# Kernel tuning notes

Measured on AMD Instinct MI355X. Metric: run time of the kernel, lower is better.

## Reference

```python
import jax, jax.numpy as jnp
import numpy as np

N_NODES = 65536
N_EDGES = 524288
IN_CH = 128
FHC = 256      # first_hc = max(hidden, in)
HID = 256
NCLS = 3
NODES_PER_GRAPH = 32


def setup_inputs() -> dict:
    key = jax.random.key(0)
    ks = jax.random.split(key, 16)
    s = 1.0 / np.sqrt(FHC)
    inp = {
        "x": jax.random.normal(ks[0], (N_NODES, IN_CH), dtype=jnp.float32),
        "edge_index": jax.random.randint(ks[1], (2, N_EDGES), 0, N_NODES, dtype=jnp.int64),
        "edge_attr": jax.random.uniform(ks[2], (N_EDGES,), dtype=jnp.float32),
        # GatedGraphConv params: per-layer matmul weight + GRUCell
        "gg_w": jax.random.uniform(ks[3], (2, FHC, FHC), minval=-s, maxval=s, dtype=jnp.float32),
        "w_ih": jax.random.uniform(ks[4], (3 * FHC, FHC), minval=-s, maxval=s, dtype=jnp.float32),
        "w_hh": jax.random.uniform(ks[5], (3 * FHC, FHC), minval=-s, maxval=s, dtype=jnp.float32),
        "b_ih": jax.random.uniform(ks[6], (3 * FHC,), minval=-s, maxval=s, dtype=jnp.float32),
        "b_hh": jax.random.uniform(ks[7], (3 * FHC,), minval=-s, maxval=s, dtype=jnp.float32),
        # Conv1d(FHC, 1, kernel_size=1)
        "cnn_w": jax.random.uniform(ks[8], (1, FHC, 1), minval=-s, maxval=s, dtype=jnp.float32),
        "cnn_b": jax.random.uniform(ks[9], (1,), minval=-s, maxval=s, dtype=jnp.float32),
        # Linear(32, HID), Linear(HID, NCLS)
        "lin1_w": jax.random.uniform(ks[10], (HID, NODES_PER_GRAPH), minval=-0.17, maxval=0.17, dtype=jnp.float32),
        "lin1_b": jax.random.uniform(ks[11], (HID,), minval=-0.17, maxval=0.17, dtype=jnp.float32),
        "lin2_w": jax.random.uniform(ks[12], (NCLS, HID), minval=-s, maxval=s, dtype=jnp.float32),
        "lin2_b": jax.random.uniform(ks[13], (NCLS,), minval=-s, maxval=s, dtype=jnp.float32),
    }
    return inp


def _gated_graph_conv(x, src, dst, edge_w, gg_w, w_ih, w_hh, b_ih, b_hh):
    # PyG GatedGraphConv: pad input to out_channels, then num_layers iterations.
    n = x.shape[0]
    h = jnp.pad(x, ((0, 0), (0, FHC - x.shape[1])))  # [N, FHC]
    for i in range(2):
        m = h @ gg_w[i]                                   # [N, FHC]
        msgs = m[src] * edge_w[:, None]                   # gather per edge [E, FHC]
        agg = jax.ops.segment_sum(msgs, dst, num_segments=n)  # scatter-add [N, FHC]
        # GRUCell(input=agg, hidden=h), torch gate order: r, z, n
        gi = agg @ w_ih.T + b_ih
        gh = h @ w_hh.T + b_hh
        ir, iz, ig = jnp.split(gi, 3, axis=1)
        hr, hz, hg = jnp.split(gh, 3, axis=1)
        r = jax.nn.sigmoid(ir + hr)
        z = jax.nn.sigmoid(iz + hz)
        g = jnp.tanh(ig + r * hg)
        h = (1.0 - z) * g + z * h
    return h


def reference(x, edge_index, edge_attr, gg_w, w_ih, w_hh, b_ih, b_hh,
              cnn_w, cnn_b, lin1_w, lin1_b, lin2_w, lin2_b):
    src, dst = edge_index[0], edge_index[1]
    h = _gated_graph_conv(x, src, dst, edge_attr, gg_w, w_ih, w_hh, b_ih, b_hh)
    h = jax.nn.relu(h)  # dropout is identity in eval mode
    bs = h.shape[0] // NODES_PER_GRAPH
    h = h.reshape(bs, NODES_PER_GRAPH, FHC)          # (bs e) f -> bs e f
    # Conv1d(FHC,1,k=1) over layout (bs, f, e): y[b,e] = sum_f w[0,f,0]*h[b,e,f] + b
    y = jnp.einsum('bef,f->be', h, cnn_w[:, :, 0].reshape(FHC)) + cnn_b[0]
    y = jax.nn.relu(y)                               # [bs, 32]
    y = y @ lin1_w.T + lin1_b
    y = jax.nn.relu(y)
    y = y @ lin2_w.T + lin2_b
    return jax.nn.softmax(y, axis=-1)
```

## Files before the change

kernel.cpp:

```cpp
#include <hip/hip_runtime.h>
#include <math.h>

#define N_NODES 65536
#define N_EDGES 524288
#define IN_CH 128
#define FHC 256
#define NCLS 3
#define NPG 32
#define NGRAPH (N_NODES / NPG)

typedef __attribute__((ext_vector_type(8))) short bfrag;
typedef __attribute__((ext_vector_type(4))) float facc;

__device__ inline float sigmoidf_(float x) { return 1.0f / (1.0f + expf(-x)); }

__device__ __forceinline__ float fast_sigmoid(float x) {
    return __builtin_amdgcn_rcpf(1.0f + __expf(-x));
}
__device__ __forceinline__ float fast_tanh(float x) {
    return 1.0f - 2.0f * __builtin_amdgcn_rcpf(__expf(2.0f * x) + 1.0f);
}

__device__ inline short f2bf(float f) {
    union { float f; unsigned u; } v; v.f = f;
    unsigned r = v.u + 0x7fffu + ((v.u >> 16) & 1u);
    return (short)(r >> 16);
}
__device__ inline float bf2f(short s) {
    union { unsigned u; float f; } v; v.u = ((unsigned)(unsigned short)s) << 16;
    return v.f;
}

__device__ __forceinline__ void gld16(const short* g, short* l) {
    __builtin_amdgcn_global_load_lds(
        (const __attribute__((address_space(1))) void*)g,
        (__attribute__((address_space(3))) void*)l, 16, 0, 0);
}

__global__ void convert_kernel(const float* __restrict__ gg_w, const float* __restrict__ wih,
                               const float* __restrict__ whh, short* __restrict__ ggT,
                               short* __restrict__ wih16, short* __restrict__ whh16) {
    int t = blockIdx.x * 256 + threadIdx.x;
    if (t < 2 * FHC * FHC) {
        int i = t >> 16, r = t & 65535, n = r >> 8, k = r & 255;
        ggT[t] = f2bf(gg_w[i * FHC * FHC + k * FHC + n]);
    } else if (t < 2 * FHC * FHC + 3 * FHC * FHC) {
        int u = t - 2 * FHC * FHC;
        wih16[u] = f2bf(wih[u]);
    } else {
        int u = t - 5 * FHC * FHC;
        whh16[u] = f2bf(whh[u]);
    }
}

__global__ void pad16_kernel(const float* __restrict__ x, short* __restrict__ h) {
    int idx = blockIdx.x * 256 + threadIdx.x;
    int c4 = idx & 63, n = idx >> 6;
    short4 v = {0, 0, 0, 0};
    if (c4 < 32) {
        float4 xv = reinterpret_cast<const float4*>(x)[n * 32 + c4];
        v.x = f2bf(xv.x); v.y = f2bf(xv.y); v.z = f2bf(xv.z); v.w = f2bf(xv.w);
    }
    reinterpret_cast<short4*>(h)[idx] = v;
}

__global__ void hist_kernel(const int* __restrict__ ei, int* __restrict__ deg) {
    int e = blockIdx.x * 256 + threadIdx.x;
    atomicAdd(&deg[ei[N_EDGES + e]], 1);
}

__global__ void scan_reduce_kernel(const int* __restrict__ deg, int* __restrict__ bsum) {
    __shared__ int s[256];
    int t = threadIdx.x;
    s[t] = deg[blockIdx.x * 256 + t];
    __syncthreads();
    for (int off = 128; off > 0; off >>= 1) {
        if (t < off) s[t] += s[t + off];
        __syncthreads();
    }
    if (t == 0) bsum[blockIdx.x] = s[0];
}

__global__ void scan_bsum_kernel(const int* __restrict__ bsum, int* __restrict__ boff) {
    __shared__ int s[256];
    int t = threadIdx.x;
    int v = bsum[t];
    s[t] = v;
    __syncthreads();
    for (int off = 1; off < 256; off <<= 1) {
        int u = (t >= off) ? s[t - off] : 0;
        __syncthreads();
        s[t] += u;
        __syncthreads();
    }
    boff[t] = s[t] - v;
}

__global__ void scan_write_kernel(const int* __restrict__ deg, const int* __restrict__ boff,
                                  int* __restrict__ rowptr, int* __restrict__ cur) {
    __shared__ int s[256];
    int t = threadIdx.x, gid = blockIdx.x * 256 + t;
    int v = deg[gid];
    s[t] = v;
    __syncthreads();
    for (int off = 1; off < 256; off <<= 1) {
        int u = (t >= off) ? s[t - off] : 0;
        __syncthreads();
        s[t] += u;
        __syncthreads();
    }
    int excl = boff[blockIdx.x] + s[t] - v;
    rowptr[gid] = excl;
    cur[gid] = excl;
    if (gid == N_NODES - 1) rowptr[N_NODES] = excl + v;
}

__global__ void fill_kernel(const int* __restrict__ ei, const float* __restrict__ ea,
                            int* __restrict__ cur, int2* __restrict__ csr) {
    int e = blockIdx.x * 256 + threadIdx.x;
    int dst = ei[N_EDGES + e];
    int pos = atomicAdd(&cur[dst], 1);
    csr[pos] = make_int2(ei[e], __float_as_int(ea[e]));
}

__global__ __launch_bounds__(256) void gather_kernel(const short* __restrict__ m,
                                                     const int* __restrict__ rowptr,
                                                     const int2* __restrict__ csr,
                                                     short* __restrict__ agg16) {
    int node = blockIdx.x * 4 + (threadIdx.x >> 6);
    int lane = threadIdx.x & 63;
    int beg = rowptr[node], end = rowptr[node + 1];
    const short4* m4 = reinterpret_cast<const short4*>(m);
    float a0 = 0.f, a1 = 0.f, a2 = 0.f, a3 = 0.f;
#define GSTEP(E)                                            \
    {                                                       \
        float w = __int_as_float((E).y);                    \
        short4 v = m4[(size_t)(E).x * 64 + lane];           \
        a0 += bf2f(v.x) * w;                                \
        a1 += bf2f(v.y) * w;                                \
        a2 += bf2f(v.z) * w;                                \
        a3 += bf2f(v.w) * w;                                \
    }
    int j = beg;
    for (; j + 8 <= end; j += 8) {
        int2 e0 = csr[j + 0], e1 = csr[j + 1], e2 = csr[j + 2], e3 = csr[j + 3];
        int2 e4 = csr[j + 4], e5 = csr[j + 5], e6 = csr[j + 6], e7 = csr[j + 7];
        GSTEP(e0) GSTEP(e1) GSTEP(e2) GSTEP(e3)
        GSTEP(e4) GSTEP(e5) GSTEP(e6) GSTEP(e7)
    }
    for (; j + 2 <= end; j += 2) {
        int2 e0 = csr[j + 0], e1 = csr[j + 1];
        GSTEP(e0) GSTEP(e1)
    }
    if (j < end) {
        int2 e0 = csr[j];
        GSTEP(e0)
    }
#undef GSTEP
    short4 o;
    o.x = f2bf(a0); o.y = f2bf(a1); o.z = f2bf(a2); o.w = f2bf(a3);
    reinterpret_cast<short4*>(agg16)[(size_t)node * 64 + lane] = o;
}

__global__ __launch_bounds__(256, 2) void mgemm_kernel(const short* __restrict__ A,
                                                       const short* __restrict__ W,
                                                       short* __restrict__ C) {
    __shared__ __align__(16) short lds[3 * 16 * 512];
    int tid = threadIdx.x;
    int lane = tid & 63, wv = tid >> 6, fr = lane & 15, fc = lane >> 4;
    int m0 = blockIdx.x * 128, n0 = blockIdx.y * 128;
    int srow = lane >> 2;
    int scol = (lane & 3) ^ ((lane >> 3) & 3);
    const short* gsrc[4];
    int ldsoff[4];
#pragma unroll
    for (int i = 0; i < 4; ++i) {
        int ch = wv * 4 + i;
        if (ch < 8) {
            ldsoff[i] = ch * 512;
            gsrc[i] = A + (size_t)(m0 + ch * 16 + srow) * FHC + scol * 8;
        } else {
            ldsoff[i] = 4096 + (ch - 8) * 512;
            gsrc[i] = W + (size_t)(n0 + (ch - 8) * 16 + srow) * FHC + scol * 8;
        }
    }
    int fcs = fc ^ ((fr >> 1) & 3);

    auto STAGE = [&](int ks, int bufsel) {
        short* dst = &lds[bufsel * 8192];
#pragma unroll
        for (int i = 0; i < 4; ++i) gld16(gsrc[i] + ks * 32, dst + ldsoff[i]);
    };

    facc acc[2][8] = {};
    STAGE(0, 0);
    STAGE(1, 1);
    for (int ks = 0; ks < 8; ++ks) {
        if (ks < 7) { asm volatile("s_waitcnt vmcnt(4)" ::: "memory"); }
        else        { asm volatile("s_waitcnt vmcnt(0)" ::: "memory"); }
        __builtin_amdgcn_sched_barrier(0);
        __builtin_amdgcn_s_barrier();
        __builtin_amdgcn_sched_barrier(0);
        if (ks + 2 < 8) STAGE(ks + 2, (ks + 2) % 3);
        __builtin_amdgcn_sched_barrier(0);
        const short* B = &lds[(ks % 3) * 8192];
        int ar = (wv * 32 + fr) * 32 + fcs * 8;
        bfrag a0 = *reinterpret_cast<const bfrag*>(B + ar);
        bfrag a1 = *reinterpret_cast<const bfrag*>(B + ar + 16 * 32);
        __builtin_amdgcn_s_setprio(1);
#pragma unroll
        for (int cf = 0; cf < 8; ++cf) {
            bfrag b = *reinterpret_cast<const bfrag*>(B + 4096 + (cf * 16 + fr) * 32 + fcs * 8);
            acc[0][cf] = __builtin_amdgcn_mfma_f32_16x16x32_bf16(a0, b, acc[0][cf], 0, 0, 0);
            acc[1][cf] = __builtin_amdgcn_mfma_f32_16x16x32_bf16(a1, b, acc[1][cf], 0, 0, 0);
        }
        __builtin_amdgcn_s_setprio(0);
    }
#pragma unroll
    for (int s = 0; s < 2; ++s)
#pragma unroll
        for (int cf = 0; cf < 8; ++cf)
#pragma unroll
            for (int r = 0; r < 4; ++r) {
                int node = m0 + wv * 32 + s * 16 + fc * 4 + r;
                int c = n0 + cf * 16 + fr;
                C[(size_t)node * FHC + c] = f2bf(acc[s][cf][r]);
            }
}

__global__ __launch_bounds__(256, 2) void gru_mfma_kernel(
    const short* __restrict__ agg16, const short* __restrict__ hin, short* __restrict__ hout,
    const short* __restrict__ wih16, const short* __restrict__ whh16,
    const float* __restrict__ bih, const float* __restrict__ bhh) {
    __shared__ __align__(16) short lds[3 * 16 * 512];
    int tid = threadIdx.x;
    int lane = tid & 63, wv = tid >> 6, fr = lane & 15, fc = lane >> 4;
    int c = blockIdx.y * 64 + wv * 16 + fr;

    bfrag wreg[6][8];
    {
        size_t roff = (size_t)c * FHC + fc * 8;
#pragma unroll
        for (int ks = 0; ks < 8; ++ks) {
            wreg[0][ks] = *reinterpret_cast<const bfrag*>(wih16 + roff + ks * 32);
            wreg[1][ks] = *reinterpret_cast<const bfrag*>(wih16 + (size_t)256 * FHC + roff + ks * 32);
            wreg[2][ks] = *reinterpret_cast<const bfrag*>(wih16 + (size_t)512 * FHC + roff + ks * 32);
            wreg[3][ks] = *reinterpret_cast<const bfrag*>(whh16 + roff + ks * 32);
            wreg[4][ks] = *reinterpret_cast<const bfrag*>(whh16 + (size_t)256 * FHC + roff + ks * 32);
            wreg[5][ks] = *reinterpret_cast<const bfrag*>(whh16 + (size_t)512 * FHC + roff + ks * 32);
        }
    }
    float br = bih[c] + bhh[c];
    float bz = bih[c + 256] + bhh[c + 256];
    float big = bih[c + 512], bhg = bhh[c + 512];

    int srow = lane >> 2;
    int scol = (lane & 3) ^ ((lane >> 3) & 3);
    const short* gb[4];
    int ldsoff[4];
#pragma unroll
    for (int i = 0; i < 4; ++i) {
        int ch = wv * 4 + i;
        int mat = ch >> 3, ks = ch & 7;
        const short* src = mat ? hin : agg16;
        gb[i] = src + (size_t)srow * FHC + ks * 32 + scol * 8;
        ldsoff[i] = ch * 512;
    }
    int fcs = fc ^ ((fr >> 1) & 3);
    int lo = (fr * 4 + fcs) * 8;
    const int NT = 32;
    int tile0 = blockIdx.x * NT;

    int hbase = (8 + (c >> 5)) * 512 + (c & 7);
    int hg = (c >> 3) & 3;

    auto STAGE = [&](int t, int bufsel) {
        size_t noff = (size_t)(tile0 + t) * 16 * FHC;
        short* dst = &lds[bufsel * 8192];
#pragma unroll
        for (int i = 0; i < 4; ++i) gld16(gb[i] + noff, dst + ldsoff[i]);
    };

    STAGE(0, 0);
    STAGE(1, 1);
    for (int t = 0; t < NT; ++t) {
        if (t == 0)                   { asm volatile("s_waitcnt vmcnt(4)" ::: "memory"); }
        else if (t == 1 || t == NT-1) { asm volatile("s_waitcnt vmcnt(8)" ::: "memory"); }
        else                          { asm volatile("s_waitcnt vmcnt(12)" ::: "memory"); }
        __builtin_amdgcn_sched_barrier(0);
        __builtin_amdgcn_s_barrier();
        __builtin_amdgcn_sched_barrier(0);
        if (t + 2 < NT) STAGE(t + 2, (t + 2) % 3);
        __builtin_amdgcn_sched_barrier(0);
        const short* B = &lds[(t % 3) * 8192];
        facc aR = {}, aZ = {}, aG = {}, aH = {};
        __builtin_amdgcn_s_setprio(1);
#pragma unroll
        for (int ks = 0; ks < 8; ++ks) {
            bfrag ag = *reinterpret_cast<const bfrag*>(B + ks * 512 + lo);
            bfrag hh = *reinterpret_cast<const bfrag*>(B + (8 + ks) * 512 + lo);
            aR = __builtin_amdgcn_mfma_f32_16x16x32_bf16(ag, wreg[0][ks], aR, 0, 0, 0);
            aR = __builtin_amdgcn_mfma_f32_16x16x32_bf16(hh, wreg[3][ks], aR, 0, 0, 0);
            aZ = __builtin_amdgcn_mfma_f32_16x16x32_bf16(ag, wreg[1][ks], aZ, 0, 0, 0);
            aZ = __builtin_amdgcn_mfma_f32_16x16x32_bf16(hh, wreg[4][ks], aZ, 0, 0, 0);
            aG = __builtin_amdgcn_mfma_f32_16x16x32_bf16(ag, wreg[2][ks], aG, 0, 0, 0);
            aH = __builtin_amdgcn_mfma_f32_16x16x32_bf16(hh, wreg[5][ks], aH, 0, 0, 0);
        }
        __builtin_amdgcn_s_setprio(0);
        int node0 = (tile0 + t) * 16;
#pragma unroll
        for (int r = 0; r < 4; ++r) {
            int row = fc * 4 + r;
            float hold = bf2f(B[hbase + (row * 4 + (hg ^ ((row >> 1) & 3))) * 8]);
            float rg = fast_sigmoid(aR[r] + br);
            float z = fast_sigmoid(aZ[r] + bz);
            float g = fast_tanh(aG[r] + big + rg * (aH[r] + bhg));
            hout[(size_t)(node0 + row) * FHC + c] = f2bf(g + z * (hold - g));
        }
    }
}

__global__ void cnn_kernel(const short* __restrict__ h, const float* __restrict__ w,
                           const float* __restrict__ b, float* __restrict__ y1) {
    int node = blockIdx.x * 4 + (threadIdx.x >> 6);
    int lane = threadIdx.x & 63;
    short4 hv = reinterpret_cast<const short4*>(h)[(size_t)node * 64 + lane];
    float4 wv = reinterpret_cast<const float4*>(w)[lane];
    float p = fmaxf(bf2f(hv.x), 0.f) * wv.x + fmaxf(bf2f(hv.y), 0.f) * wv.y +
              fmaxf(bf2f(hv.z), 0.f) * wv.z + fmaxf(bf2f(hv.w), 0.f) * wv.w;
#pragma unroll
    for (int off = 32; off > 0; off >>= 1) p += __shfl_down(p, off, 64);
    if (lane == 0) y1[node] = fmaxf(p + b[0], 0.f);
}

__global__ __launch_bounds__(256) void head_kernel(
    const float* __restrict__ y1, const float* __restrict__ l1w,
    const float* __restrict__ l1b, const float* __restrict__ l2w,
    const float* __restrict__ l2b, float* __restrict__ out) {
    __shared__ float ys[32];
    __shared__ float zs[256];
    __shared__ float os[3];
    int b = blockIdx.x, tid = threadIdx.x;
    if (tid < 32) ys[tid] = y1[b * 32 + tid];
    __syncthreads();
    float acc = l1b[tid];
#pragma unroll
    for (int k = 0; k < 32; ++k) acc += ys[k] * l1w[tid * 32 + k];
    zs[tid] = fmaxf(acc, 0.f);
    __syncthreads();
    int wave = tid >> 6, lane = tid & 63;
    if (wave < 3) {
        float p = 0.f;
#pragma unroll
        for (int j = 0; j < 4; ++j) p += zs[lane + j * 64] * l2w[wave * 256 + lane + j * 64];
#pragma unroll
        for (int off = 32; off > 0; off >>= 1) p += __shfl_down(p, off, 64);
        if (lane == 0) os[wave] = p + l2b[wave];
    }
    __syncthreads();
    if (tid == 0) {
        float mx = fmaxf(os[0], fmaxf(os[1], os[2]));
        float e0 = expf(os[0] - mx), e1 = expf(os[1] - mx), e2 = expf(os[2] - mx);
        float s = e0 + e1 + e2;
        out[b * 3 + 0] = e0 / s;
        out[b * 3 + 1] = e1 / s;
        out[b * 3 + 2] = e2 / s;
    }
}

extern "C" void kernel_launch(void* const* d_in, const int* in_sizes, int n_in,
                              void* d_out, int out_size, void* d_ws, size_t ws_size,
                              hipStream_t stream) {
    const float* x = (const float*)d_in[0];
    const int* ei = (const int*)d_in[1];
    const float* ea = (const float*)d_in[2];
    const float* gg_w = (const float*)d_in[3];
    const float* w_ih = (const float*)d_in[4];
    const float* w_hh = (const float*)d_in[5];
    const float* b_ih = (const float*)d_in[6];
    const float* b_hh = (const float*)d_in[7];
    const float* cnn_w = (const float*)d_in[8];
    const float* cnn_b = (const float*)d_in[9];
    const float* l1w = (const float*)d_in[10];
    const float* l1b = (const float*)d_in[11];
    const float* l2w = (const float*)d_in[12];
    const float* l2b = (const float*)d_in[13];
    float* out = (float*)d_out;

    const size_t nodeE = (size_t)N_NODES * FHC;
    char* p = (char*)d_ws;
    short* hA = (short*)p;      p += nodeE * 2;
    short* hB = (short*)p;      p += nodeE * 2;
    short* m16 = (short*)p;     p += nodeE * 2;
    short* agg16 = (short*)p;   p += nodeE * 2;
    short* ggT = (short*)p;     p += (size_t)2 * FHC * FHC * 2;
    short* wih16 = (short*)p;   p += (size_t)3 * FHC * FHC * 2;
    short* whh16 = (short*)p;   p += (size_t)3 * FHC * FHC * 2;
    float* y1 = (float*)p;      p += (size_t)N_NODES * 4;
    int* deg = (int*)p;         p += (size_t)N_NODES * 4;
    int* rowptr = (int*)p;      p += (size_t)(N_NODES + 4) * 4;
    int* cur = (int*)p;         p += (size_t)N_NODES * 4;
    int* bsum = (int*)p;        p += 256 * 4;
    int* boff = (int*)p;        p += 256 * 4;
    int2* csr = (int2*)p;       p += (size_t)N_EDGES * 8;

    dim3 grid_gemm(N_NODES / 128, FHC / 128);
    dim3 grid_gru(128, 4);

    convert_kernel<<<8 * FHC * FHC / 256, 256, 0, stream>>>(gg_w, w_ih, w_hh, ggT, wih16, whh16);
    pad16_kernel<<<N_NODES * 64 / 256, 256, 0, stream>>>(x, hA);

    hipMemsetAsync(deg, 0, (size_t)N_NODES * 4, stream);
    hist_kernel<<<N_EDGES / 256, 256, 0, stream>>>(ei, deg);
    scan_reduce_kernel<<<N_NODES / 256, 256, 0, stream>>>(deg, bsum);
    scan_bsum_kernel<<<1, 256, 0, stream>>>(bsum, boff);
    scan_write_kernel<<<N_NODES / 256, 256, 0, stream>>>(deg, boff, rowptr, cur);
    fill_kernel<<<N_EDGES / 256, 256, 0, stream>>>(ei, ea, cur, csr);

    mgemm_kernel<<<grid_gemm, 256, 0, stream>>>(hA, ggT, m16);
    gather_kernel<<<N_NODES / 4, 256, 0, stream>>>(m16, rowptr, csr, agg16);
    gru_mfma_kernel<<<grid_gru, 256, 0, stream>>>(agg16, hA, hB, wih16, whh16, b_ih, b_hh);

    mgemm_kernel<<<grid_gemm, 256, 0, stream>>>(hB, ggT + FHC * FHC, m16);
    gather_kernel<<<N_NODES / 4, 256, 0, stream>>>(m16, rowptr, csr, agg16);
    gru_mfma_kernel<<<grid_gru, 256, 0, stream>>>(agg16, hB, hA, wih16, whh16, b_ih, b_hh);

    cnn_kernel<<<N_NODES / 4, 256, 0, stream>>>(hA, cnn_w, cnn_b, y1);
    head_kernel<<<NGRAPH, 256, 0, stream>>>(y1, l1w, l1b, l2w, l2b, out);
}
```

Before: 319.7 us.

## Software-pipeline GRU epilogue with next tile's MFMA using ping-pong accumulators

The GRU tile loop is restructured so the gate nonlinearities and h stores for tile t-1 run after the MFMA chain for tile t, using two alternating accumulator sets. The aim is to hide transcendental math and global store latency behind matrix-core work. The old h values are read from LDS into registers during the current tile, so the buffer can be recycled. This costs extra VGPRs for the second accumulator set, retunes the vmcnt waits and drops the setprio hints.

```diff
diff --git a/kernel.cpp b/kernel.cpp
--- a/kernel.cpp
+++ b/kernel.cpp
@@ -281,41 +281,73 @@
         for (int i = 0; i < 4; ++i) gld16(gb[i] + noff, dst + ldsoff[i]);
     };
 
+    facc aR0 = {}, aZ0 = {}, aG0 = {}, aH0 = {};
+    facc aR1 = {}, aZ1 = {}, aG1 = {}, aH1 = {};
+    float hd0[4], hd1[4];
+    const facc FZ = {0.f, 0.f, 0.f, 0.f};
+
     STAGE(0, 0);
     STAGE(1, 1);
-    for (int t = 0; t < NT; ++t) {
-        if (t == 0)                   { asm volatile("s_waitcnt vmcnt(4)" ::: "memory"); }
-        else if (t == 1 || t == NT-1) { asm volatile("s_waitcnt vmcnt(8)" ::: "memory"); }
-        else                          { asm volatile("s_waitcnt vmcnt(12)" ::: "memory"); }
-        __builtin_amdgcn_sched_barrier(0);
-        __builtin_amdgcn_s_barrier();
-        __builtin_amdgcn_sched_barrier(0);
-        if (t + 2 < NT) STAGE(t + 2, (t + 2) % 3);
-        __builtin_amdgcn_sched_barrier(0);
-        const short* B = &lds[(t % 3) * 8192];
-        facc aR = {}, aZ = {}, aG = {}, aH = {};
-        __builtin_amdgcn_s_setprio(1);
-#pragma unroll
-        for (int ks = 0; ks < 8; ++ks) {
-            bfrag ag = *reinterpret_cast<const bfrag*>(B + ks * 512 + lo);
-            bfrag hh = *reinterpret_cast<const bfrag*>(B + (8 + ks) * 512 + lo);
-            aR = __builtin_amdgcn_mfma_f32_16x16x32_bf16(ag, wreg[0][ks], aR, 0, 0, 0);
-            aR = __builtin_amdgcn_mfma_f32_16x16x32_bf16(hh, wreg[3][ks], aR, 0, 0, 0);
-            aZ = __builtin_amdgcn_mfma_f32_16x16x32_bf16(ag, wreg[1][ks], aZ, 0, 0, 0);
-            aZ = __builtin_amdgcn_mfma_f32_16x16x32_bf16(hh, wreg[4][ks], aZ, 0, 0, 0);
-            aG = __builtin_amdgcn_mfma_f32_16x16x32_bf16(ag, wreg[2][ks], aG, 0, 0, 0);
-            aH = __builtin_amdgcn_mfma_f32_16x16x32_bf16(hh, wreg[5][ks], aH, 0, 0, 0);
-        }
-        __builtin_amdgcn_s_setprio(0);
-        int node0 = (tile0 + t) * 16;
+
+#define GRU_TILE(T, aRc, aZc, aGc, aHc, hdc, aRp, aZp, aGp, aHp, hdp, FIRST)                 \
+    do {                                                                                     \
+        int t_ = (T);                                                                        \
+        if (t_ <= 1)            { asm volatile("s_waitcnt vmcnt(4)" ::: "memory"); }         \
+        else if (t_ == 2)       { asm volatile("s_waitcnt vmcnt(8)" ::: "memory"); }         \
+        else if (t_ == NT - 1)  { asm volatile("s_waitcnt vmcnt(8)" ::: "memory"); }         \
+        else                    { asm volatile("s_waitcnt vmcnt(12)" ::: "memory"); }        \
+        __builtin_amdgcn_sched_barrier(0);                                                   \
+        __builtin_amdgcn_s_barrier();                                                        \
+        __builtin_amdgcn_sched_barrier(0);                                                   \
+        if (t_ + 2 < NT) STAGE(t_ + 2, (t_ + 2) % 3);                                        \
+        const short* B = &lds[(t_ % 3) * 8192];                                              \
+        aRc = FZ; aZc = FZ; aGc = FZ; aHc = FZ;                                              \
+        _Pragma("unroll")                                                                    \
+        for (int ks = 0; ks < 8; ++ks) {                                                     \
+            bfrag ag = *reinterpret_cast<const bfrag*>(B + ks * 512 + lo);                   \
+            bfrag hh = *reinterpret_cast<const bfrag*>(B + (8 + ks) * 512 + lo);             \
+            aRc = __builtin_amdgcn_mfma_f32_16x16x32_bf16(ag, wreg[0][ks], aRc, 0, 0, 0);    \
+            aRc = __builtin_amdgcn_mfma_f32_16x16x32_bf16(hh, wreg[3][ks], aRc, 0, 0, 0);    \
+            aZc = __builtin_amdgcn_mfma_f32_16x16x32_bf16(ag, wreg[1][ks], aZc, 0, 0, 0);    \
+            aZc = __builtin_amdgcn_mfma_f32_16x16x32_bf16(hh, wreg[4][ks], aZc, 0, 0, 0);    \
+            aGc = __builtin_amdgcn_mfma_f32_16x16x32_bf16(ag, wreg[2][ks], aGc, 0, 0, 0);    \
+            aHc = __builtin_amdgcn_mfma_f32_16x16x32_bf16(hh, wreg[5][ks], aHc, 0, 0, 0);    \
+        }                                                                                    \
+        _Pragma("unroll")                                                                    \
+        for (int r = 0; r < 4; ++r) {                                                        \
+            int row = fc * 4 + r;                                                            \
+            hdc[r] = bf2f(B[hbase + (row * 4 + (hg ^ ((row >> 1) & 3))) * 8]);               \
+        }                                                                                    \
+        if (!(FIRST)) {                                                                      \
+            int node0 = (tile0 + t_ - 1) * 16;                                               \
+            _Pragma("unroll")                                                                \
+            for (int r = 0; r < 4; ++r) {                                                    \
+                int row = fc * 4 + r;                                                        \
+                float rg = fast_sigmoid(aRp[r] + br);                                        \
+                float z = fast_sigmoid(aZp[r] + bz);                                         \
+                float g = fast_tanh(aGp[r] + big + rg * (aHp[r] + bhg));                     \
+                hout[(size_t)(node0 + row) * FHC + c] = f2bf(g + z * (hdp[r] - g));          \
+            }                                                                                \
+        }                                                                                    \
+        __builtin_amdgcn_sched_barrier(0);                                                   \
+    } while (0)
+
+    GRU_TILE(0, aR0, aZ0, aG0, aH0, hd0, aR1, aZ1, aG1, aH1, hd1, true);
+    GRU_TILE(1, aR1, aZ1, aG1, aH1, hd1, aR0, aZ0, aG0, aH0, hd0, false);
+    for (int tt = 2; tt < NT; tt += 2) {
+        GRU_TILE(tt, aR0, aZ0, aG0, aH0, hd0, aR1, aZ1, aG1, aH1, hd1, false);
+        GRU_TILE(tt + 1, aR1, aZ1, aG1, aH1, hd1, aR0, aZ0, aG0, aH0, hd0, false);
+    }
+#undef GRU_TILE
+    {
+        int node0 = (tile0 + NT - 1) * 16;
 #pragma unroll
         for (int r = 0; r < 4; ++r) {
             int row = fc * 4 + r;
-            float hold = bf2f(B[hbase + (row * 4 + (hg ^ ((row >> 1) & 3))) * 8]);
-            float rg = fast_sigmoid(aR[r] + br);
-            float z = fast_sigmoid(aZ[r] + bz);
-            float g = fast_tanh(aG[r] + big + rg * (aH[r] + bhg));
-            hout[(size_t)(node0 + row) * FHC + c] = f2bf(g + z * (hold - g));
+            float rg = fast_sigmoid(aR1[r] + br);
+            float z = fast_sigmoid(aZ1[r] + bz);
+            float g = fast_tanh(aG1[r] + big + rg * (aH1[r] + bhg));
+            hout[(size_t)(node0 + row) * FHC + c] = f2bf(g + z * (hd1[r] - g));
         }
     }
 }
```

Result: slower. 524.8 us (+64.1%).

## Fold message weight into GRU input weight and gather raw hidden states

Applied to the files above, without the earlier changes.

The code reassociates (A·(h·W))·W_ihᵀ as (A·h)·(W·W_ihᵀ). Two small weight products are precomputed once, so the per-node message GEMM and its intermediate buffer disappear from both layers. The gather now aggregates h directly, and the GRU kernel consumes the fused weight. The first layer runs a templated variant that only walks the 128 non-padded input channels, halving its K loop and staging. In exchange, the fused weight is rounded to bf16 once, so numerics differ slightly, and the code adds templated wait counts and special handling for the padded hidden columns.

```diff
diff --git a/kernel.cpp b/kernel.cpp
--- a/kernel.cpp
+++ b/kernel.cpp
@@ -12,8 +12,6 @@
 typedef __attribute__((ext_vector_type(8))) short bfrag;
 typedef __attribute__((ext_vector_type(4))) float facc;
 
-__device__ inline float sigmoidf_(float x) { return 1.0f / (1.0f + expf(-x)); }
-
 __device__ __forceinline__ float fast_sigmoid(float x) {
     return __builtin_amdgcn_rcpf(1.0f + __expf(-x));
 }
@@ -37,14 +35,23 @@
         (__attribute__((address_space(3))) void*)l, 16, 0, 0);
 }
 
+template <int N> __device__ __forceinline__ void vwait() {
+    if constexpr (N == 0)       asm volatile("s_waitcnt vmcnt(0)" ::: "memory");
+    else if constexpr (N == 2)  asm volatile("s_waitcnt vmcnt(2)" ::: "memory");
+    else if constexpr (N == 4)  asm volatile("s_waitcnt vmcnt(4)" ::: "memory");
+    else if constexpr (N == 6)  asm volatile("s_waitcnt vmcnt(6)" ::: "memory");
+    else if constexpr (N == 8)  asm volatile("s_waitcnt vmcnt(8)" ::: "memory");
+    else if constexpr (N == 10) asm volatile("s_waitcnt vmcnt(10)" ::: "memory");
+    else                        asm volatile("s_waitcnt vmcnt(12)" ::: "memory");
+}
+
 __global__ void convert_kernel(const float* __restrict__ gg_w, const float* __restrict__ wih,
-                               const float* __restrict__ whh, short* __restrict__ ggT,
+                               const float* __restrict__ whh, short* __restrict__ gg16,
                                short* __restrict__ wih16, short* __restrict__ whh16) {
     int t = blockIdx.x * 256 + threadIdx.x;
     if (t < 2 * FHC * FHC) {
-        int i = t >> 16, r = t & 65535, n = r >> 8, k = r & 255;
-        ggT[t] = f2bf(gg_w[i * FHC * FHC + k * FHC + n]);
-    } else if (t < 2 * FHC * FHC + 3 * FHC * FHC) {
+        gg16[t] = f2bf(gg_w[t]);
+    } else if (t < 5 * FHC * FHC) {
         int u = t - 2 * FHC * FHC;
         wih16[u] = f2bf(wih[u]);
     } else {
@@ -228,23 +235,27 @@
             }
 }
 
-__global__ __launch_bounds__(256, 2) void gru_mfma_kernel(
-    const short* __restrict__ agg16, const short* __restrict__ hin, short* __restrict__ hout,
-    const short* __restrict__ wih16, const short* __restrict__ whh16,
+template <int NKS>
+__global__ __launch_bounds__(256, 2) void gru_fused_kernel(
+    const short* __restrict__ hagg16, const short* __restrict__ hin, short* __restrict__ hout,
+    const short* __restrict__ wfT, const short* __restrict__ whh16,
     const float* __restrict__ bih, const float* __restrict__ bhh) {
-    __shared__ __align__(16) short lds[3 * 16 * 512];
+    constexpr int NCH = 2 * NKS;
+    constexpr int NL = NCH / 4;
+    constexpr int BUF = NCH * 512;
+    __shared__ __align__(16) short lds[3 * BUF];
     int tid = threadIdx.x;
     int lane = tid & 63, wv = tid >> 6, fr = lane & 15, fc = lane >> 4;
     int c = blockIdx.y * 64 + wv * 16 + fr;
 
-    bfrag wreg[6][8];
+    bfrag wreg[6][NKS];
     {
         size_t roff = (size_t)c * FHC + fc * 8;
 #pragma unroll
-        for (int ks = 0; ks < 8; ++ks) {
-            wreg[0][ks] = *reinterpret_cast<const bfrag*>(wih16 + roff + ks * 32);
-            wreg[1][ks] = *reinterpret_cast<const bfrag*>(wih16 + (size_t)256 * FHC + roff + ks * 32);
-            wreg[2][ks] = *reinterpret_cast<const bfrag*>(wih16 + (size_t)512 * FHC + roff + ks * 32);
+        for (int ks = 0; ks < NKS; ++ks) {
+            wreg[0][ks] = *reinterpret_cast<const bfrag*>(wfT + roff + ks * 32);
+            wreg[1][ks] = *reinterpret_cast<const bfrag*>(wfT + (size_t)256 * FHC + roff + ks * 32);
+            wreg[2][ks] = *reinterpret_cast<const bfrag*>(wfT + (size_t)512 * FHC + roff + ks * 32);
             wreg[3][ks] = *reinterpret_cast<const bfrag*>(whh16 + roff + ks * 32);
             wreg[4][ks] = *reinterpret_cast<const bfrag*>(whh16 + (size_t)256 * FHC + roff + ks * 32);
             wreg[5][ks] = *reinterpret_cast<const bfrag*>(whh16 + (size_t)512 * FHC + roff + ks * 32);
@@ -256,13 +267,13 @@
 
     int srow = lane >> 2;
     int scol = (lane & 3) ^ ((lane >> 3) & 3);
-    const short* gb[4];
-    int ldsoff[4];
-#pragma unroll
-    for (int i = 0; i < 4; ++i) {
-        int ch = wv * 4 + i;
-        int mat = ch >> 3, ks = ch & 7;
-        const short* src = mat ? hin : agg16;
+    const short* gb[NL];
+    int ldsoff[NL];
+#pragma unroll
+    for (int i = 0; i < NL; ++i) {
+        int ch = wv * NL + i;
+        int ks = ch & (NKS - 1);
+        const short* src = (ch >= NKS) ? hin : hagg16;
         gb[i] = src + (size_t)srow * FHC + ks * 32 + scol * 8;
         ldsoff[i] = ch * 512;
     }
@@ -271,34 +282,37 @@
     const int NT = 32;
     int tile0 = blockIdx.x * NT;
 
-    int hbase = (8 + (c >> 5)) * 512 + (c & 7);
-    int hg = (c >> 3) & 3;
+    int cc = (NKS == 4 && c >= 128) ? 0 : c;
+    int hbase = (NKS + (cc >> 5)) * 512 + (cc & 7);
+    int hg = (cc >> 3) & 3;
+    bool hvalid = (NKS == 8) || (c < 128);
 
     auto STAGE = [&](int t, int bufsel) {
         size_t noff = (size_t)(tile0 + t) * 16 * FHC;
-        short* dst = &lds[bufsel * 8192];
-#pragma unroll
-        for (int i = 0; i < 4; ++i) gld16(gb[i] + noff, dst + ldsoff[i]);
+        short* dst = &lds[bufsel * BUF];
+#pragma unroll
+        for (int i = 0; i < NL; ++i) gld16(gb[i] + noff, dst + ldsoff[i]);
     };
 
     STAGE(0, 0);
     STAGE(1, 1);
     for (int t = 0; t < NT; ++t) {
-        if (t == 0)                   { asm volatile("s_waitcnt vmcnt(4)" ::: "memory"); }
-        else if (t == 1 || t == NT-1) { asm volatile("s_waitcnt vmcnt(8)" ::: "memory"); }
-        else                          { asm volatile("s_waitcnt vmcnt(12)" ::: "memory"); }
+        if (t == 0)           vwait<NL>();
+        else if (t == 1)      vwait<NL + 4>();
+        else if (t == NT - 1) vwait<8>();
+        else                  vwait<NL + 8>();
         __builtin_amdgcn_sched_barrier(0);
         __builtin_amdgcn_s_barrier();
         __builtin_amdgcn_sched_barrier(0);
         if (t + 2 < NT) STAGE(t + 2, (t + 2) % 3);
         __builtin_amdgcn_sched_barrier(0);
-        const short* B = &lds[(t % 3) * 8192];
+        const short* B = &lds[(t % 3) * BUF];
         facc aR = {}, aZ = {}, aG = {}, aH = {};
         __builtin_amdgcn_s_setprio(1);
 #pragma unroll
-        for (int ks = 0; ks < 8; ++ks) {
+        for (int ks = 0; ks < NKS; ++ks) {
             bfrag ag = *reinterpret_cast<const bfrag*>(B + ks * 512 + lo);
-            bfrag hh = *reinterpret_cast<const bfrag*>(B + (8 + ks) * 512 + lo);
+            bfrag hh = *reinterpret_cast<const bfrag*>(B + (NKS + ks) * 512 + lo);
             aR = __builtin_amdgcn_mfma_f32_16x16x32_bf16(ag, wreg[0][ks], aR, 0, 0, 0);
             aR = __builtin_amdgcn_mfma_f32_16x16x32_bf16(hh, wreg[3][ks], aR, 0, 0, 0);
             aZ = __builtin_amdgcn_mfma_f32_16x16x32_bf16(ag, wreg[1][ks], aZ, 0, 0, 0);
@@ -311,7 +325,7 @@
 #pragma unroll
         for (int r = 0; r < 4; ++r) {
             int row = fc * 4 + r;
-            float hold = bf2f(B[hbase + (row * 4 + (hg ^ ((row >> 1) & 3))) * 8]);
+            float hold = hvalid ? bf2f(B[hbase + (row * 4 + (hg ^ ((row >> 1) & 3))) * 8]) : 0.f;
             float rg = fast_sigmoid(aR[r] + br);
             float z = fast_sigmoid(aZ[r] + bz);
             float g = fast_tanh(aG[r] + big + rg * (aH[r] + bhg));
@@ -391,11 +405,12 @@
     char* p = (char*)d_ws;
     short* hA = (short*)p;      p += nodeE * 2;
     short* hB = (short*)p;      p += nodeE * 2;
-    short* m16 = (short*)p;     p += nodeE * 2;
-    short* agg16 = (short*)p;   p += nodeE * 2;
-    short* ggT = (short*)p;     p += (size_t)2 * FHC * FHC * 2;
+    short* hagg = (short*)p;    p += nodeE * 2;
+    short* gg16 = (short*)p;    p += (size_t)2 * FHC * FHC * 2;
     short* wih16 = (short*)p;   p += (size_t)3 * FHC * FHC * 2;
     short* whh16 = (short*)p;   p += (size_t)3 * FHC * FHC * 2;
+    short* wfT0 = (short*)p;    p += (size_t)3 * FHC * FHC * 2;
+    short* wfT1 = (short*)p;    p += (size_t)3 * FHC * FHC * 2;
     float* y1 = (float*)p;      p += (size_t)N_NODES * 4;
     int* deg = (int*)p;         p += (size_t)N_NODES * 4;
     int* rowptr = (int*)p;      p += (size_t)(N_NODES + 4) * 4;
@@ -404,11 +419,14 @@
     int* boff = (int*)p;        p += 256 * 4;
     int2* csr = (int2*)p;       p += (size_t)N_EDGES * 8;
 
-    dim3 grid_gemm(N_NODES / 128, FHC / 128);
+    dim3 grid_wf(768 / 128, 256 / 128);
     dim3 grid_gru(128, 4);
 
-    convert_kernel<<<8 * FHC * FHC / 256, 256, 0, stream>>>(gg_w, w_ih, w_hh, ggT, wih16, whh16);
+    convert_kernel<<<8 * FHC * FHC / 256, 256, 0, stream>>>(gg_w, w_ih, w_hh, gg16, wih16, whh16);
     pad16_kernel<<<N_NODES * 64 / 256, 256, 0, stream>>>(x, hA);
+
+    mgemm_kernel<<<grid_wf, 256, 0, stream>>>(wih16, gg16, wfT0);
+    mgemm_kernel<<<grid_wf, 256, 0, stream>>>(wih16, gg16 + FHC * FHC, wfT1);
 
     hipMemsetAsync(deg, 0, (size_t)N_NODES * 4, stream);
     hist_kernel<<<N_EDGES / 256, 256, 0, stream>>>(ei, deg);
@@ -417,13 +435,11 @@
     scan_write_kernel<<<N_NODES / 256, 256, 0, stream>>>(deg, boff, rowptr, cur);
     fill_kernel<<<N_EDGES / 256, 256, 0, stream>>>(ei, ea, cur, csr);
 
-    mgemm_kernel<<<grid_gemm, 256, 0, stream>>>(hA, ggT, m16);
-    gather_kernel<<<N_NODES / 4, 256, 0, stream>>>(m16, rowptr, csr, agg16);
-    gru_mfma_kernel<<<grid_gru, 256, 0, stream>>>(agg16, hA, hB, wih16, whh16, b_ih, b_hh);
-
-    mgemm_kernel<<<grid_gemm, 256, 0, stream>>>(hB, ggT + FHC * FHC, m16);
-    gather_kernel<<<N_NODES / 4, 256, 0, stream>>>(m16, rowptr, csr, agg16);
-    gru_mfma_kernel<<<grid_gru, 256, 0, stream>>>(agg16, hB, hA, wih16, whh16, b_ih, b_hh);
+    gather_kernel<<<N_NODES / 4, 256, 0, stream>>>(hA, rowptr, csr, hagg);
+    gru_fused_kernel<4><<<grid_gru, 256, 0, stream>>>(hagg, hA, hB, wfT0, whh16, b_ih, b_hh);
+
+    gather_kernel<<<N_NODES / 4, 256, 0, stream>>>(hB, rowptr, csr, hagg);
+    gru_fused_kernel<8><<<grid_gru, 256, 0, stream>>>(hagg, hB, hA, wfT1, whh16, b_ih, b_hh);
 
     cnn_kernel<<<N_NODES / 4, 256, 0, stream>>>(hA, cnn_w, cnn_b, y1);
     head_kernel<<<NGRAPH, 256, 0, stream>>>(y1, l1w, l1b, l2w, l2b, out);
```

Result: faster. 276.6 us (-13.5%).
